# Optimization experiments

Hardware: AMD Instinct MI355X
Metric: run time of the kernel (lower is better)

## Reference

```python
import jax, jax.numpy as jnp
import numpy as np
from jax import lax

HEIGHT, WIDTH = 13, 10
HIDDEN = 256
CONV_OUT = 32 * 3 * 2  # 192, matches torch _get_conv_output_size


def setup_inputs() -> dict:
    key = jax.random.key(0)
    ks = jax.random.split(key, 12)
    B, T = 128, 512
    s = 0.05
    return {
        "x": jax.random.normal(ks[0], (B, T, HEIGHT, WIDTH), jnp.float32),
        "conv1_w": jax.random.normal(ks[1], (16, 1, 3, 3), jnp.float32) * s,
        "conv1_b": jax.random.normal(ks[2], (16,), jnp.float32) * s,
        "conv2_w": jax.random.normal(ks[3], (32, 16, 3, 3), jnp.float32) * s,
        "conv2_b": jax.random.normal(ks[4], (32,), jnp.float32) * s,
        "W_ih": jax.random.normal(ks[5], (4 * HIDDEN, CONV_OUT), jnp.float32) * s,
        "b_ih": jax.random.normal(ks[6], (4 * HIDDEN,), jnp.float32) * s,
        "W_hh": jax.random.normal(ks[7], (4 * HIDDEN, HIDDEN), jnp.float32) * s,
        "b_hh": jax.random.normal(ks[8], (4 * HIDDEN,), jnp.float32) * s,
        "cls_w": jax.random.normal(ks[9], (64, HIDDEN), jnp.float32) * s,
        "cls_b": jax.random.normal(ks[10], (64,), jnp.float32) * s,
    }


def _conv2d(x, w, b):
    # NCHW, OIHW, padding=1 (SAME for 3x3)
    y = lax.conv_general_dilated(x, w, window_strides=(1, 1),
                                 padding=((1, 1), (1, 1)),
                                 dimension_numbers=("NCHW", "OIHW", "NCHW"))
    return y + b[None, :, None, None]


def _maxpool2(x):
    # kernel 2, stride 2, VALID (floor) like nn.MaxPool2d(2)
    return lax.reduce_window(x, -jnp.inf, lax.max,
                             (1, 1, 2, 2), (1, 1, 2, 2), "VALID")


def reference(x, conv1_w, conv1_b, conv2_w, conv2_b, W_ih, b_ih, W_hh, b_hh, cls_w, cls_b):
    B, T, Hd, Wd = x.shape
    xi = x.reshape(B * T, 1, Hd, Wd)
    y = _maxpool2(jax.nn.relu(_conv2d(xi, conv1_w, conv1_b)))
    y = _maxpool2(jax.nn.relu(_conv2d(y, conv2_w, conv2_b)))
    feat = y.reshape(B, T, -1)  # [B, T, 192], channel-major flatten matches torch view

    # Precompute input contribution to gates for all steps (same math, batched)
    gx_all = jnp.einsum("btf,gf->btg", feat, W_ih) + b_ih + b_hh  # [B, T, 4H]
    H = W_hh.shape[1]

    def step(carry, gx):
        h, c = carry
        gates = gx + h @ W_hh.T  # [B, 4H]
        i, f, g, o = jnp.split(gates, 4, axis=1)
        i = jax.nn.sigmoid(i)
        f = jax.nn.sigmoid(f)
        g = jnp.tanh(g)
        o = jax.nn.sigmoid(o)
        c = f * c + i * g
        h = o * jnp.tanh(c)
        return (h, c), None

    h0 = jnp.zeros((B, H), x.dtype)
    c0 = jnp.zeros((B, H), x.dtype)
    (hT, _), _ = lax.scan(step, (h0, c0), jnp.swapaxes(gx_all, 0, 1))
    logits = hT @ cls_w.T + cls_b
    return logits
```

## Files before the change

### kernel.cpp

```cpp
#include <hip/hip_runtime.h>
#include <hip/hip_bf16.h>


typedef _Float16 half2v __attribute__((ext_vector_type(2)));
typedef _Float16 f16x8 __attribute__((ext_vector_type(8)));
typedef float f32x4 __attribute__((ext_vector_type(4)));

__device__ __forceinline__ float dot2f16(half2v a, half2v b, float c) {
#if defined(__has_builtin)
#if __has_builtin(__builtin_amdgcn_fdot2)
    return __builtin_amdgcn_fdot2(a, b, c, false);
#else
    return c + (float)a.x * (float)b.x + (float)a.y * (float)b.y;
#endif
#else
    return c + (float)a.x * (float)b.x + (float)a.y * (float)b.y;
#endif
}

__device__ __forceinline__ unsigned int packf2(const float* p) {
    half2v hv;
    hv.x = (_Float16)p[0];
    hv.y = (_Float16)p[1];
    return __builtin_bit_cast(unsigned int, hv);
}

__device__ __forceinline__ half2v bch2(unsigned int u) {
    return __builtin_bit_cast(half2v, u);
}

__device__ __forceinline__ uint4 pack8(const float* p) {
    uint4 v;
    v.x = packf2(p + 0);
    v.y = packf2(p + 2);
    v.z = packf2(p + 4);
    v.w = packf2(p + 6);
    return v;
}

__global__ __launch_bounds__(256) void prepack_kernel(
    const float* __restrict__ Whh, uint4* __restrict__ sw)
{
    int idx = blockIdx.x * 256 + threadIdx.x;
    if (idx < 13 * 1024) {
        int c = idx >> 10, r = idx & 1023;
        sw[idx] = pack8(Whh + (size_t)r * 256 + 152 + 8 * c);
    }
}

__global__ __launch_bounds__(256) void conv_kernel(
    const float* __restrict__ x,
    const float* __restrict__ c1w,
    const float* __restrict__ c1b,
    const float* __restrict__ c2w,
    const float* __restrict__ c2b,
    _Float16* __restrict__ feat)
{
    __shared__ float w1t[9 * 16];
    __shared__ float b1s[16];
    __shared__ float w2t[16 * 9 * 32];
    __shared__ float b2s[32];
    __shared__ float xp[4][14 * 12];
    __shared__ float p1p[4][16 * 8 * 7];

    const int tid = threadIdx.x;

    for (int idx = tid; idx < 144; idx += 256) {
        int oc = idx / 9, k = idx % 9;
        w1t[k * 16 + oc] = c1w[idx];
    }
    if (tid < 16) b1s[tid] = c1b[tid];
    for (int idx = tid; idx < 4608; idx += 256) {
        int oc = idx / 144, ic = (idx / 9) % 16, k = idx % 9;
        w2t[(ic * 9 + k) * 32 + oc] = c2w[idx];
    }
    if (tid < 32) b2s[tid] = c2b[tid];

    const int w = tid >> 6;
    const int lane = tid & 63;
    const int img = blockIdx.x * 4 + w;

    for (int i = lane; i < 14 * 12; i += 64) xp[w][i] = 0.f;
    for (int i = lane; i < 16 * 8 * 7; i += 64) p1p[w][i] = 0.f;
    __syncthreads();

    const float* xin = x + (size_t)img * 130;
    for (int i = lane; i < 130; i += 64) {
        int r = i / 10, c = i % 10;
        xp[w][(r + 1) * 12 + (c + 1)] = xin[i];
    }
    __syncthreads();

    {
        const int oc = lane & 15, q = lane >> 4;
        #pragma unroll
        for (int i = 0; i < 8; i++) {
            int pos = i * 4 + q;
            if (pos < 30) {
                int ph = pos / 5, pw = pos % 5;
                float cmax = -1e30f;
                #pragma unroll
                for (int pt = 0; pt < 4; pt++) {
                    int Y = 2 * ph + (pt >> 1), X = 2 * pw + (pt & 1);
                    float s = 0.f;
                    #pragma unroll
                    for (int k = 0; k < 9; k++) {
                        int dy = k / 3, dx = k % 3;
                        s += w1t[k * 16 + oc] * xp[w][(Y + dy) * 12 + X + dx];
                    }
                    cmax = fmaxf(cmax, s);
                }
                p1p[w][(oc * 8 + ph + 1) * 7 + (pw + 1)] = fmaxf(0.f, cmax + b1s[oc]);
            }
        }
    }
    __syncthreads();

    {
        const int oc = lane & 31, pw2 = lane >> 5;
        float acc[3][4];
        #pragma unroll
        for (int a = 0; a < 3; a++)
            #pragma unroll
            for (int b = 0; b < 4; b++) acc[a][b] = 0.f;

        for (int ic = 0; ic < 16; ic++) {
            #pragma unroll
            for (int k = 0; k < 9; k++) {
                int dy = k / 3, dx = k % 3;
                float wv = w2t[(ic * 9 + k) * 32 + oc];
                #pragma unroll
                for (int ph2 = 0; ph2 < 3; ph2++) {
                    #pragma unroll
                    for (int pt = 0; pt < 4; pt++) {
                        int y = 2 * ph2 + (pt >> 1) + dy;
                        int xx = 2 * pw2 + (pt & 1) + dx;
                        acc[ph2][pt] += wv * p1p[w][(ic * 8 + y) * 7 + xx];
                    }
                }
            }
        }
        float bias = b2s[oc];
        _Float16* fo = feat + (size_t)img * 192;
        #pragma unroll
        for (int ph2 = 0; ph2 < 3; ph2++) {
            float m = fmaxf(fmaxf(acc[ph2][0], acc[ph2][1]),
                            fmaxf(acc[ph2][2], acc[ph2][3]));
            fo[oc * 6 + ph2 * 2 + pw2] = (_Float16)fmaxf(0.f, m + bias);
        }
    }
}

__global__ __launch_bounds__(256) void gemm_gx_kernel(
    const _Float16* __restrict__ feat,
    const float* __restrict__ Wih,
    const float* __restrict__ bih,
    const float* __restrict__ bhh,
    _Float16* __restrict__ gx)
{
    __shared__ uint4 As4[64][25];
    __shared__ uint4 Bs4[64][25];

    const int tid = threadIdx.x;
    const int n0 = blockIdx.x * 64;
    const int m0 = blockIdx.y * 64;

    #pragma unroll
    for (int it = 0; it < 6; it++) {
        int q = tid + it * 256;
        int m = q / 24, c = q % 24;
        As4[m][c] = *(const uint4*)(feat + (size_t)(m0 + m) * 192 + c * 8);
    }
    unsigned int* Bu = (unsigned int*)Bs4;
    #pragma unroll
    for (int it = 0; it < 24; it++) {
        int q = tid + it * 256;
        int n = q / 96, p = q % 96;
        Bu[n * 100 + p] = packf2(Wih + (size_t)(n0 + n) * 192 + 2 * p);
    }
    __syncthreads();

    const int wv = tid >> 6;
    const int lane = tid & 63;
    const int lm = lane & 15;
    const int lk = lane >> 4;

    f32x4 acc[4] = {{0.f, 0.f, 0.f, 0.f}, {0.f, 0.f, 0.f, 0.f},
                    {0.f, 0.f, 0.f, 0.f}, {0.f, 0.f, 0.f, 0.f}};

    #pragma unroll
    for (int ks = 0; ks < 6; ks++) {
        f16x8 a = __builtin_bit_cast(f16x8, As4[wv * 16 + lm][ks * 4 + lk]);
        #pragma unroll
        for (int j = 0; j < 4; j++) {
            f16x8 b = __builtin_bit_cast(f16x8, Bs4[j * 16 + lm][ks * 4 + lk]);
            acc[j] = __builtin_amdgcn_mfma_f32_16x16x32_f16(a, b, acc[j], 0, 0, 0);
        }
    }

    #pragma unroll
    for (int j = 0; j < 4; j++) {
        int n = n0 + j * 16 + lm;
        float bias = bih[n] + bhh[n];
        #pragma unroll
        for (int i = 0; i < 4; i++) {
            int m = m0 + wv * 16 + lk * 4 + i;
            gx[(size_t)m * 1024 + n] = (_Float16)(acc[j][i] + bias);
        }
    }
}

__global__ __launch_bounds__(512, 2) void lstm_kernel(
    const _Float16* __restrict__ gx,
    const float* __restrict__ Whh,
    const uint4* __restrict__ sw,
    const float* __restrict__ clsw,
    const float* __restrict__ clsb,
    float* __restrict__ out)
{
    __shared__ uint4 wl4[9][1024];
    __shared__ __align__(16) _Float16 hbuf[2][256];
    __shared__ float xg[512];

    const int t = threadIdx.x;
    const int b = blockIdx.x;
    const int r0 = t, r1 = t + 512;

    const float* w0 = Whh + (size_t)r0 * 256;
    const float* w1 = Whh + (size_t)r1 * 256;

    #pragma unroll
    for (int ch = 0; ch < 9; ch++) {
        wl4[ch][r0] = pack8(w0 + 8 * ch);
        wl4[ch][r1] = pack8(w1 + 8 * ch);
    }
    half2v wr0[40], wr1[40];
    #pragma unroll
    for (int q = 0; q < 40; q++) {
        wr0[q] = bch2(packf2(w0 + 72 + 2 * q));
        wr1[q] = bch2(packf2(w1 + 72 + 2 * q));
    }
    if (t < 256) hbuf[0][t] = (_Float16)0.f;
    __syncthreads();

    float c = 0.f;
    int cur = 0;
    const _Float16* gxb = gx + (size_t)b * 512 * 1024;
    float ga = (float)gxb[r0];
    float gb = (float)gxb[r1];

    for (int step = 0; step < 512; step++) {
        const _Float16* gxn = gxb + (size_t)((step + 1) & 511) * 1024;
        _Float16 na = gxn[r0];
        _Float16 nb = gxn[r1];

        float acc0 = ga, acc1 = gb;
        const uint4* hb4 = (const uint4*)&hbuf[cur][0];

        #pragma unroll
        for (int sc = 0; sc < 13; sc++) {
            uint4 u0 = sw[sc * 1024 + r0];
            uint4 u1 = sw[sc * 1024 + r1];
            uint4 hv = hb4[19 + sc];
            acc0 = dot2f16(bch2(u0.x), bch2(hv.x), acc0);
            acc0 = dot2f16(bch2(u0.y), bch2(hv.y), acc0);
            acc0 = dot2f16(bch2(u0.z), bch2(hv.z), acc0);
            acc0 = dot2f16(bch2(u0.w), bch2(hv.w), acc0);
            acc1 = dot2f16(bch2(u1.x), bch2(hv.x), acc1);
            acc1 = dot2f16(bch2(u1.y), bch2(hv.y), acc1);
            acc1 = dot2f16(bch2(u1.z), bch2(hv.z), acc1);
            acc1 = dot2f16(bch2(u1.w), bch2(hv.w), acc1);
        }
        #pragma unroll
        for (int ch = 0; ch < 9; ch++) {
            uint4 u0 = wl4[ch][r0];
            uint4 u1 = wl4[ch][r1];
            uint4 hv = hb4[ch];
            acc0 = dot2f16(bch2(u0.x), bch2(hv.x), acc0);
            acc0 = dot2f16(bch2(u0.y), bch2(hv.y), acc0);
            acc0 = dot2f16(bch2(u0.z), bch2(hv.z), acc0);
            acc0 = dot2f16(bch2(u0.w), bch2(hv.w), acc0);
            acc1 = dot2f16(bch2(u1.x), bch2(hv.x), acc1);
            acc1 = dot2f16(bch2(u1.y), bch2(hv.y), acc1);
            acc1 = dot2f16(bch2(u1.z), bch2(hv.z), acc1);
            acc1 = dot2f16(bch2(u1.w), bch2(hv.w), acc1);
        }
        #pragma unroll
        for (int cc = 0; cc < 10; cc++) {
            uint4 hv = hb4[9 + cc];
            acc0 = dot2f16(wr0[4 * cc + 0], bch2(hv.x), acc0);
            acc0 = dot2f16(wr0[4 * cc + 1], bch2(hv.y), acc0);
            acc0 = dot2f16(wr0[4 * cc + 2], bch2(hv.z), acc0);
            acc0 = dot2f16(wr0[4 * cc + 3], bch2(hv.w), acc0);
            acc1 = dot2f16(wr1[4 * cc + 0], bch2(hv.x), acc1);
            acc1 = dot2f16(wr1[4 * cc + 1], bch2(hv.y), acc1);
            acc1 = dot2f16(wr1[4 * cc + 2], bch2(hv.z), acc1);
            acc1 = dot2f16(wr1[4 * cc + 3], bch2(hv.w), acc1);
        }

        if (t >= 256) {
            xg[t - 256] = acc0;
            xg[t] = acc1;
        }
        __syncthreads();
        if (t < 256) {
            float i_ = 1.f / (1.f + __expf(-acc0));
            float g_ = 1.f - 2.f / (__expf(2.f * acc1) + 1.f);
            float f_ = 1.f / (1.f + __expf(-xg[t]));
            float o_ = 1.f / (1.f + __expf(-xg[t + 256]));
            c = f_ * c + i_ * g_;
            float th = 1.f - 2.f / (__expf(2.f * c) + 1.f);
            float h = o_ * th;
            hbuf[cur ^ 1][t] = (_Float16)h;
        }
        __syncthreads();
        cur ^= 1;
        ga = (float)na;
        gb = (float)nb;
    }

    if (t < 64) {
        const float* cw = clsw + t * 256;
        float s = clsb[t];
        for (int k = 0; k < 256; k++) s += cw[k] * (float)hbuf[cur][k];
        out[b * 64 + t] = s;
    }
}

extern "C" void kernel_launch(void* const* d_in, const int* in_sizes, int n_in,
                              void* d_out, int out_size, void* d_ws, size_t ws_size,
                              hipStream_t stream) {
    const float* x    = (const float*)d_in[0];
    const float* c1w  = (const float*)d_in[1];
    const float* c1b  = (const float*)d_in[2];
    const float* c2w  = (const float*)d_in[3];
    const float* c2b  = (const float*)d_in[4];
    const float* Wih  = (const float*)d_in[5];
    const float* bih  = (const float*)d_in[6];
    const float* Whh  = (const float*)d_in[7];
    const float* bhh  = (const float*)d_in[8];
    const float* clsw = (const float*)d_in[9];
    const float* clsb = (const float*)d_in[10];

    _Float16* feat = (_Float16*)d_ws;
    _Float16* gx   = feat + (size_t)65536 * 192;
    uint4* sw      = (uint4*)(gx + (size_t)65536 * 1024);
    float* outp = (float*)d_out;

    hipLaunchKernelGGL(prepack_kernel, dim3(52), dim3(256), 0, stream, Whh, sw);
    hipLaunchKernelGGL(conv_kernel, dim3(16384), dim3(256), 0, stream,
                       x, c1w, c1b, c2w, c2b, feat);
    hipLaunchKernelGGL(gemm_gx_kernel, dim3(16, 1024), dim3(256), 0, stream,
                       feat, Wih, bih, bhh, gx);
    hipLaunchKernelGGL(lstm_kernel, dim3(128), dim3(512), 0, stream,
                       gx, Whh, sw, clsw, clsb, outp);
}
```

Baseline: 1.293 ms.

## Prepack W_ih to fp16 and enlarge gx GEMM tiles to 128x128

Adds a prepack kernel that converts W_ih to fp16 once, so GEMM blocks load fp16 tiles directly instead of converting fp32 weights in every block. The GEMM tile grows from 64x64 to 128x128, with each wave computing a 32x128 strip using 16 MFMA accumulators, and gx is written as packed 4-half stores. The workspace region is reused: W_ih fp16 is staged there first, then overwritten by the W_hh prepack before the LSTM kernel runs. The larger tiles raise register and LDS pressure and cut the block count.

```diff
diff --git a/kernel.cpp b/kernel.cpp
--- a/kernel.cpp
+++ b/kernel.cpp
@@ -38,7 +38,14 @@
     return v;
 }
 
-__global__ __launch_bounds__(256) void prepack_kernel(
+__global__ __launch_bounds__(256) void prepack_w_kernel(
+    const float* __restrict__ Wih, uint4* __restrict__ wf)
+{
+    int idx = blockIdx.x * 256 + threadIdx.x;
+    if (idx < 1024 * 192 / 8) wf[idx] = pack8(Wih + idx * 8);
+}
+
+__global__ __launch_bounds__(256) void prepack_sw_kernel(
     const float* __restrict__ Whh, uint4* __restrict__ sw)
 {
     int idx = blockIdx.x * 256 + threadIdx.x;
@@ -151,61 +158,68 @@
     }
 }
 
-__global__ __launch_bounds__(256) void gemm_gx_kernel(
+__global__ __launch_bounds__(256, 1) void gemm_gx_kernel(
     const _Float16* __restrict__ feat,
-    const float* __restrict__ Wih,
+    const _Float16* __restrict__ wf16,
     const float* __restrict__ bih,
     const float* __restrict__ bhh,
     _Float16* __restrict__ gx)
 {
-    __shared__ uint4 As4[64][25];
-    __shared__ uint4 Bs4[64][25];
+    __shared__ uint4 As4[128][25];
+    __shared__ uint4 Ws4[128][25];
 
     const int tid = threadIdx.x;
-    const int n0 = blockIdx.x * 64;
-    const int m0 = blockIdx.y * 64;
-
-    #pragma unroll
-    for (int it = 0; it < 6; it++) {
+    const int n0 = blockIdx.x * 128;
+    const int m0 = blockIdx.y * 128;
+
+    #pragma unroll
+    for (int it = 0; it < 12; it++) {
         int q = tid + it * 256;
-        int m = q / 24, c = q % 24;
-        As4[m][c] = *(const uint4*)(feat + (size_t)(m0 + m) * 192 + c * 8);
-    }
-    unsigned int* Bu = (unsigned int*)Bs4;
-    #pragma unroll
-    for (int it = 0; it < 24; it++) {
-        int q = tid + it * 256;
-        int n = q / 96, p = q % 96;
-        Bu[n * 100 + p] = packf2(Wih + (size_t)(n0 + n) * 192 + 2 * p);
-    }
-    __syncthreads();
-
-    const int wv = tid >> 6;
+        int r = q / 24, c = q % 24;
+        As4[r][c] = *(const uint4*)(feat + (size_t)(m0 + r) * 192 + c * 8);
+        Ws4[r][c] = *(const uint4*)(wf16 + (size_t)(n0 + r) * 192 + c * 8);
+    }
+    __syncthreads();
+
+    const int w = tid >> 6;
     const int lane = tid & 63;
     const int lm = lane & 15;
     const int lk = lane >> 4;
 
-    f32x4 acc[4] = {{0.f, 0.f, 0.f, 0.f}, {0.f, 0.f, 0.f, 0.f},
-                    {0.f, 0.f, 0.f, 0.f}, {0.f, 0.f, 0.f, 0.f}};
-
+    f32x4 acc[2][8] = {};
     #pragma unroll
     for (int ks = 0; ks < 6; ks++) {
-        f16x8 a = __builtin_bit_cast(f16x8, As4[wv * 16 + lm][ks * 4 + lk]);
-        #pragma unroll
-        for (int j = 0; j < 4; j++) {
-            f16x8 b = __builtin_bit_cast(f16x8, Bs4[j * 16 + lm][ks * 4 + lk]);
-            acc[j] = __builtin_amdgcn_mfma_f32_16x16x32_f16(a, b, acc[j], 0, 0, 0);
-        }
-    }
-
-    #pragma unroll
-    for (int j = 0; j < 4; j++) {
-        int n = n0 + j * 16 + lm;
-        float bias = bih[n] + bhh[n];
-        #pragma unroll
-        for (int i = 0; i < 4; i++) {
-            int m = m0 + wv * 16 + lk * 4 + i;
-            gx[(size_t)m * 1024 + n] = (_Float16)(acc[j][i] + bias);
+        f16x8 wf[2], af[8];
+        #pragma unroll
+        for (int nf = 0; nf < 2; nf++)
+            wf[nf] = __builtin_bit_cast(f16x8, Ws4[w * 32 + nf * 16 + lm][ks * 4 + lk]);
+        #pragma unroll
+        for (int mf = 0; mf < 8; mf++)
+            af[mf] = __builtin_bit_cast(f16x8, As4[mf * 16 + lm][ks * 4 + lk]);
+        #pragma unroll
+        for (int nf = 0; nf < 2; nf++)
+            #pragma unroll
+            for (int mf = 0; mf < 8; mf++)
+                acc[nf][mf] = __builtin_amdgcn_mfma_f32_16x16x32_f16(
+                    wf[nf], af[mf], acc[nf][mf], 0, 0, 0);
+    }
+
+    #pragma unroll
+    for (int nf = 0; nf < 2; nf++) {
+        int nb = n0 + w * 32 + nf * 16 + lk * 4;
+        float4 b1 = *(const float4*)&bih[nb];
+        float4 b2 = *(const float4*)&bhh[nb];
+        float bs0 = b1.x + b2.x, bs1 = b1.y + b2.y;
+        float bs2 = b1.z + b2.z, bs3 = b1.w + b2.w;
+        #pragma unroll
+        for (int mf = 0; mf < 8; mf++) {
+            int m = m0 + mf * 16 + lm;
+            union { _Float16 h[4]; uint2 u; } pk;
+            pk.h[0] = (_Float16)(acc[nf][mf][0] + bs0);
+            pk.h[1] = (_Float16)(acc[nf][mf][1] + bs1);
+            pk.h[2] = (_Float16)(acc[nf][mf][2] + bs2);
+            pk.h[3] = (_Float16)(acc[nf][mf][3] + bs3);
+            *(uint2*)&gx[(size_t)m * 1024 + nb] = pk.u;
         }
     }
 }
@@ -344,14 +358,15 @@
 
     _Float16* feat = (_Float16*)d_ws;
     _Float16* gx   = feat + (size_t)65536 * 192;
-    uint4* sw      = (uint4*)(gx + (size_t)65536 * 1024);
+    uint4* aux     = (uint4*)(gx + (size_t)65536 * 1024);
     float* outp = (float*)d_out;
 
-    hipLaunchKernelGGL(prepack_kernel, dim3(52), dim3(256), 0, stream, Whh, sw);
+    hipLaunchKernelGGL(prepack_w_kernel, dim3(96), dim3(256), 0, stream, Wih, aux);
     hipLaunchKernelGGL(conv_kernel, dim3(16384), dim3(256), 0, stream,
                        x, c1w, c1b, c2w, c2b, feat);
-    hipLaunchKernelGGL(gemm_gx_kernel, dim3(16, 1024), dim3(256), 0, stream,
-                       feat, Wih, bih, bhh, gx);
+    hipLaunchKernelGGL(gemm_gx_kernel, dim3(8, 512), dim3(256), 0, stream,
+                       feat, (const _Float16*)aux, bih, bhh, gx);
+    hipLaunchKernelGGL(prepack_sw_kernel, dim3(52), dim3(256), 0, stream, Whh, aux);
     hipLaunchKernelGGL(lstm_kernel, dim3(128), dim3(512), 0, stream,
-                       gx, Whh, sw, clsw, clsb, outp);
-}
+                       gx, Whh, aux, clsw, clsb, outp);
+}
```

Measured after the change: 1.293 ms. About the same (-0.0%).
